# Kernel optimization log

Measured on AMD Instinct MI355X. Metric: run time of the kernel, lower is better.

## Reference

```python
import jax, jax.numpy as jnp
import numpy as np

EPS = 1e-7
ROUTING_ITERS = 3

def squash(s, axis=-1):
    # v = (|s|^2 / (1+|s|^2)) * s / |s|
    sq = jnp.sum(jnp.square(s), axis=axis, keepdims=True)
    return (sq / (1.0 + sq)) * s / jnp.sqrt(sq + EPS)

def setup_inputs() -> dict:
    key = jax.random.key(0)
    k1, k2 = jax.random.split(key)
    B, NI, DI = 64, 2048, 8      # batch, input capsules, input capsule dim
    NC, DC = 32, 16              # output capsules, output capsule dim
    x = jax.random.normal(k1, (B, NI, DI), dtype=jnp.float32)
    W = jax.random.normal(k2, (NC, NI, DC, DI), dtype=jnp.float32) * 0.05
    return {"x": x, "W": W}

def reference(x, W):
    # x: [B, NI, DI], W: [NC, NI, DC, DI]
    # tf.einsum('iabc,abdc->iabd') == project each input capsule per output capsule
    u = jnp.einsum('bif,cidf->bcid', x, W)          # [B, NC, NI, DC]
    B, NC, NI, DC = u.shape
    b = jnp.zeros((B, NC, NI, 1), dtype=u.dtype)
    v = None
    for _ in range(ROUTING_ITERS):
        c = jax.nn.softmax(b, axis=1)                # coupling over output capsules
        s = jnp.sum(c * u, axis=2, keepdims=True)    # [B, NC, 1, DC]
        v = squash(s, axis=-1)                       # [B, NC, 1, DC]
        # original: reduce_sum(matmul(u, tile(v)^T), axis=3) == NI * <u_i, v>
        agree = jnp.sum(u * v, axis=-1, keepdims=True)  # [B, NC, NI, 1]
        b = b + NI * agree
    return jnp.squeeze(v, axis=2)                    # [B, NC, DC]
```

## Files before the change

### kernel.cpp

```cpp
#include <hip/hip_runtime.h>

#define NI 2048
#define NB 64
#define NC 32
#define DC 16
#define DI 8

static constexpr float SQ_EPS = 1e-7f;

typedef float f8 __attribute__((ext_vector_type(8)));

template <int MODE>
__global__
__attribute__((amdgpu_flat_work_group_size(256, 256), amdgpu_waves_per_eu(2, 2)))
void route_pass(
    const float* __restrict__ x, const float* __restrict__ W,
    const float* __restrict__ veff, float* __restrict__ partial)
{
    __shared__ float4 wbuf[2112];

    const int tid   = threadIdx.x;
    const int wave  = tid >> 6;
    const int lane  = tid & 63;
    const int c     = lane & 31;
    const int dg    = lane >> 5;
    const int brel0 = wave * 4;
    const int b0    = blockIdx.y * 16 + brel0;

    f8 s0 = {}, s1 = {}, s2 = {}, s3 = {};

    f8 va = {}, vb = {}, vc = {}, vd = {};
    if (MODE == 1) {
        va = *reinterpret_cast<const f8*>(veff + (((size_t)(b0+0)*2 + dg)*32 + c)*8);
        vb = *reinterpret_cast<const f8*>(veff + (((size_t)(b0+1)*2 + dg)*32 + c)*8);
        vc = *reinterpret_cast<const f8*>(veff + (((size_t)(b0+2)*2 + dg)*32 + c)*8);
        vd = *reinterpret_cast<const f8*>(veff + (((size_t)(b0+3)*2 + dg)*32 + c)*8);
    }

    for (int rnd = 0; rnd < 8; ++rnd) {
        const int i0 = blockIdx.x * 16 + rnd * 2;
        __syncthreads();
        {
            const int k   = tid & 31;
            const int p0  = tid >> 5;
            const int k10 = k & 15, kdg = k >> 4;
#pragma unroll
            for (int r = 0; r < 8; ++r) {
                const int row = r * 8 + p0;
                const int cc  = row >> 1;
                const int sub = row & 1;
                wbuf[((sub * 16 + k10) * 2 + kdg) * 33 + cc] =
                    reinterpret_cast<const float4*>(W)[
                        ((size_t)cc * NI + i0 + sub) * 32 + k];
            }
        }
        __syncthreads();

#pragma unroll
        for (int il = 0; il < 2; ++il) {
            const f8 xav = *reinterpret_cast<const f8*>(
                x + ((size_t)(b0+0) * NI + i0 + il) * 8);
            const f8 xbv = *reinterpret_cast<const f8*>(
                x + ((size_t)(b0+1) * NI + i0 + il) * 8);
            const f8 xcv = *reinterpret_cast<const f8*>(
                x + ((size_t)(b0+2) * NI + i0 + il) * 8);
            const f8 xdv = *reinterpret_cast<const f8*>(
                x + ((size_t)(b0+3) * NI + i0 + il) * 8);

            f8 u0 = {}, u1 = {}, u2 = {}, u3 = {};
#pragma unroll
            for (int dd = 0; dd < 8; ++dd) {
                const float4 wl = wbuf[((il*16 + dd*2    )*2 + dg)*33 + c];
                const float4 wh = wbuf[((il*16 + dd*2 + 1)*2 + dg)*33 + c];
                u0[dd] = wl.x*xav[0] + wl.y*xav[1] + wl.z*xav[2] + wl.w*xav[3]
                       + wh.x*xav[4] + wh.y*xav[5] + wh.z*xav[6] + wh.w*xav[7];
                u1[dd] = wl.x*xbv[0] + wl.y*xbv[1] + wl.z*xbv[2] + wl.w*xbv[3]
                       + wh.x*xbv[4] + wh.y*xbv[5] + wh.z*xbv[6] + wh.w*xbv[7];
                u2[dd] = wl.x*xcv[0] + wl.y*xcv[1] + wl.z*xcv[2] + wl.w*xcv[3]
                       + wh.x*xcv[4] + wh.y*xcv[5] + wh.z*xcv[6] + wh.w*xcv[7];
                u3[dd] = wl.x*xdv[0] + wl.y*xdv[1] + wl.z*xdv[2] + wl.w*xdv[3]
                       + wh.x*xdv[4] + wh.y*xdv[5] + wh.z*xdv[6] + wh.w*xdv[7];
            }

            if (MODE == 0) {
                const float cu = 1.0f / 32.0f;
                s0 += u0 * cu; s1 += u1 * cu; s2 += u2 * cu; s3 += u3 * cu;
            } else {
#pragma unroll
                for (int pr = 0; pr < 2; ++pr) {
                    const f8& ue = pr ? u2 : u0;
                    const f8& uo = pr ? u3 : u1;
                    const f8& ve = pr ? vc : va;
                    const f8& vo = pr ? vd : vb;
                    float pe = 0.0f, po = 0.0f;
#pragma unroll
                    for (int k = 0; k < 8; ++k) {
                        pe += ue[k] * ve[k];
                        po += uo[k] * vo[k];
                    }
                    const float send = (dg == 0) ? po : pe;
                    const float recv = __shfl_xor(send, 32);
                    float a = ((dg == 0) ? pe : po) + recv;
                    float m = a;
#pragma unroll
                    for (int off = 16; off >= 1; off >>= 1)
                        m = fmaxf(m, __shfl_xor(m, off));
                    const float e = __expf(a - m);
                    float t = e;
#pragma unroll
                    for (int off = 16; off >= 1; off >>= 1)
                        t += __shfl_xor(t, off);
                    const float mine  = e / t;
                    const float other = __shfl_xor(mine, 32);
                    const float ce = (dg == 0) ? mine : other;
                    const float co = (dg == 0) ? other : mine;
                    if (pr == 0) { s0 += u0 * ce; s1 += u1 * co; }
                    else         { s2 += u2 * ce; s3 += u3 * co; }
                }
            }
        }
    }

    {
        const int pblk = blockIdx.y * gridDim.x + blockIdx.x;
        float* gp = partial +
            (((size_t)pblk * 16 + brel0) * 128 + dg * 64 + c * 2) * 4;
        *reinterpret_cast<f8*>(gp)        = s0;
        *reinterpret_cast<f8*>(gp +  512) = s1;
        *reinterpret_cast<f8*>(gp + 1024) = s2;
        *reinterpret_cast<f8*>(gp + 1536) = s3;
    }
}

__global__ __launch_bounds__(512) void reduce_squash(
    const float* __restrict__ partial, float* __restrict__ veff,
    float* __restrict__ out, int phase)
{
    __shared__ float4 red[512];
    const int b   = blockIdx.x;
    const int sub = threadIdx.x & 127;
    const int ibq = threadIdx.x >> 7;
    const int c   = (sub >> 2) & 31;
    const int dq  = sub & 3;

    const float* base = partial
        + ((size_t)(b >> 4) * 2048 + (b & 15)) * 512
        + (dq >> 1) * 256 + c * 8 + (dq & 1) * 4
        + (size_t)ibq * 32 * 8192;
    float4 acc = make_float4(0.f, 0.f, 0.f, 0.f);
#pragma unroll 8
    for (int ib = 0; ib < 32; ++ib) {
        const float4 p = *reinterpret_cast<const float4*>(base + (size_t)ib * 8192);
        acc.x += p.x; acc.y += p.y; acc.z += p.z; acc.w += p.w;
    }
    red[threadIdx.x] = acc;
    __syncthreads();
    if (threadIdx.x < 128) {
        const float4 a1 = red[sub + 128];
        const float4 a2 = red[sub + 256];
        const float4 a3 = red[sub + 384];
        acc.x += a1.x + a2.x + a3.x;
        acc.y += a1.y + a2.y + a3.y;
        acc.z += a1.z + a2.z + a3.z;
        acc.w += a1.w + a2.w + a3.w;

        float sq = acc.x*acc.x + acc.y*acc.y + acc.z*acc.z + acc.w*acc.w;
        sq += __shfl_xor(sq, 1);
        sq += __shfl_xor(sq, 2);
        const float scale = sq / ((1.0f + sq) * sqrtf(sq + SQ_EPS));

        if (phase == 3) {
            float4* op = reinterpret_cast<float4*>(out + ((size_t)b * NC + c) * DC + dq * 4);
            *op = make_float4(scale*acc.x, scale*acc.y, scale*acc.z, scale*acc.w);
        } else {
            const float ns = scale * (float)NI;
            float4* vp = reinterpret_cast<float4*>(
                veff + (((size_t)b * 2 + (dq >> 1)) * 32 + c) * 8 + (dq & 1) * 4);
            if (phase == 1) {
                *vp = make_float4(ns*acc.x, ns*acc.y, ns*acc.z, ns*acc.w);
            } else {
                float4 old = *vp;
                *vp = make_float4(old.x + ns*acc.x, old.y + ns*acc.y,
                                  old.z + ns*acc.z, old.w + ns*acc.w);
            }
        }
    }
}

extern "C" void kernel_launch(void* const* d_in, const int* in_sizes, int n_in,
                              void* d_out, int out_size, void* d_ws, size_t ws_size,
                              hipStream_t stream) {
    (void)in_sizes; (void)n_in; (void)out_size; (void)ws_size;
    const float* x = (const float*)d_in[0];
    const float* W = (const float*)d_in[1];

    float* partial = (float*)d_ws;
    float* veff    = (float*)d_out;

    const dim3 grid(128, 4);

    route_pass<0><<<grid, 256, 0, stream>>>(x, W, nullptr, partial);
    reduce_squash<<<64, 512, 0, stream>>>(partial, veff, nullptr, 1);

    route_pass<1><<<grid, 256, 0, stream>>>(x, W, veff, partial);
    reduce_squash<<<64, 512, 0, stream>>>(partial, veff, nullptr, 2);

    route_pass<1><<<grid, 256, 0, stream>>>(x, W, veff, partial);
    reduce_squash<<<64, 512, 0, stream>>>(partial, nullptr, (float*)d_out, 3);
}
```

Baseline: 220.9 us.

## Read W directly from global memory and stage x tile in LDS

The route pass no longer stages the W tile through a padded LDS buffer with per-round barriers. Each lane now reads its 64 W floats per input capsule straight from global memory as 32-byte vectors. The 16x16 block of x vectors is loaded once into LDS and shared by all waves. This removes eight barrier/LDS-transpose rounds, at the cost of uncoalesced strided W reads: each lane touches a different output-capsule row, so every wave load spans many cache lines. Occupancy hints are also relaxed.

```diff
diff --git a/kernel.cpp b/kernel.cpp
--- a/kernel.cpp
+++ b/kernel.cpp
@@ -12,12 +12,12 @@
 
 template <int MODE>
 __global__
-__attribute__((amdgpu_flat_work_group_size(256, 256), amdgpu_waves_per_eu(2, 2)))
+__attribute__((amdgpu_flat_work_group_size(256, 256), amdgpu_waves_per_eu(1, 2)))
 void route_pass(
     const float* __restrict__ x, const float* __restrict__ W,
     const float* __restrict__ veff, float* __restrict__ partial)
 {
-    __shared__ float4 wbuf[2112];
+    __shared__ f8 xbuf[256];
 
     const int tid   = threadIdx.x;
     const int wave  = tid >> 6;
@@ -26,6 +26,7 @@
     const int dg    = lane >> 5;
     const int brel0 = wave * 4;
     const int b0    = blockIdx.y * 16 + brel0;
+    const int i0    = blockIdx.x * 16;
 
     f8 s0 = {}, s1 = {}, s2 = {}, s3 = {};
 
@@ -37,86 +38,74 @@
         vd = *reinterpret_cast<const f8*>(veff + (((size_t)(b0+3)*2 + dg)*32 + c)*8);
     }
 
-    for (int rnd = 0; rnd < 8; ++rnd) {
-        const int i0 = blockIdx.x * 16 + rnd * 2;
-        __syncthreads();
-        {
-            const int k   = tid & 31;
-            const int p0  = tid >> 5;
-            const int k10 = k & 15, kdg = k >> 4;
+    {
+        float4* xb4 = reinterpret_cast<float4*>(xbuf);
+        const float4* xg = reinterpret_cast<const float4*>(x);
+        const int t0 = tid, t1 = tid + 256;
+        xb4[t0] = xg[((size_t)(blockIdx.y*16 + (t0>>5)) * NI + i0)*2 + (t0&31)];
+        xb4[t1] = xg[((size_t)(blockIdx.y*16 + (t1>>5)) * NI + i0)*2 + (t1&31)];
+    }
+    __syncthreads();
+
+    const float* wbase = W + ((size_t)c * NI + i0) * 128 + dg * 64;
+
+#pragma unroll 2
+    for (int ii = 0; ii < 16; ++ii) {
+        const float* wp = wbase + (size_t)ii * 128;
+        const f8 xa = xbuf[(brel0+0)*16 + ii];
+        const f8 xb = xbuf[(brel0+1)*16 + ii];
+        const f8 xc = xbuf[(brel0+2)*16 + ii];
+        const f8 xd = xbuf[(brel0+3)*16 + ii];
+
+        f8 u0 = {}, u1 = {}, u2 = {}, u3 = {};
 #pragma unroll
-            for (int r = 0; r < 8; ++r) {
-                const int row = r * 8 + p0;
-                const int cc  = row >> 1;
-                const int sub = row & 1;
-                wbuf[((sub * 16 + k10) * 2 + kdg) * 33 + cc] =
-                    reinterpret_cast<const float4*>(W)[
-                        ((size_t)cc * NI + i0 + sub) * 32 + k];
+        for (int dd = 0; dd < 8; ++dd) {
+            const f8 wv = *reinterpret_cast<const f8*>(wp + dd * 8);
+            float a0 = 0.f, a1 = 0.f, a2 = 0.f, a3 = 0.f;
+#pragma unroll
+            for (int j = 0; j < 8; ++j) {
+                a0 += wv[j] * xa[j];
+                a1 += wv[j] * xb[j];
+                a2 += wv[j] * xc[j];
+                a3 += wv[j] * xd[j];
             }
+            u0[dd] = a0; u1[dd] = a1; u2[dd] = a2; u3[dd] = a3;
         }
-        __syncthreads();
 
+        if (MODE == 0) {
+            const float cu = 1.0f / 32.0f;
+            s0 += u0 * cu; s1 += u1 * cu; s2 += u2 * cu; s3 += u3 * cu;
+        } else {
 #pragma unroll
-        for (int il = 0; il < 2; ++il) {
-            const f8 xav = *reinterpret_cast<const f8*>(
-                x + ((size_t)(b0+0) * NI + i0 + il) * 8);
-            const f8 xbv = *reinterpret_cast<const f8*>(
-                x + ((size_t)(b0+1) * NI + i0 + il) * 8);
-            const f8 xcv = *reinterpret_cast<const f8*>(
-                x + ((size_t)(b0+2) * NI + i0 + il) * 8);
-            const f8 xdv = *reinterpret_cast<const f8*>(
-                x + ((size_t)(b0+3) * NI + i0 + il) * 8);
-
-            f8 u0 = {}, u1 = {}, u2 = {}, u3 = {};
+            for (int pr = 0; pr < 2; ++pr) {
+                const f8& ue = pr ? u2 : u0;
+                const f8& uo = pr ? u3 : u1;
+                const f8& ve = pr ? vc : va;
+                const f8& vo = pr ? vd : vb;
+                float pe = 0.0f, po = 0.0f;
 #pragma unroll
-            for (int dd = 0; dd < 8; ++dd) {
-                const float4 wl = wbuf[((il*16 + dd*2    )*2 + dg)*33 + c];
-                const float4 wh = wbuf[((il*16 + dd*2 + 1)*2 + dg)*33 + c];
-                u0[dd] = wl.x*xav[0] + wl.y*xav[1] + wl.z*xav[2] + wl.w*xav[3]
-                       + wh.x*xav[4] + wh.y*xav[5] + wh.z*xav[6] + wh.w*xav[7];
-                u1[dd] = wl.x*xbv[0] + wl.y*xbv[1] + wl.z*xbv[2] + wl.w*xbv[3]
-                       + wh.x*xbv[4] + wh.y*xbv[5] + wh.z*xbv[6] + wh.w*xbv[7];
-                u2[dd] = wl.x*xcv[0] + wl.y*xcv[1] + wl.z*xcv[2] + wl.w*xcv[3]
-                       + wh.x*xcv[4] + wh.y*xcv[5] + wh.z*xcv[6] + wh.w*xcv[7];
-                u3[dd] = wl.x*xdv[0] + wl.y*xdv[1] + wl.z*xdv[2] + wl.w*xdv[3]
-                       + wh.x*xdv[4] + wh.y*xdv[5] + wh.z*xdv[6] + wh.w*xdv[7];
-            }
-
-            if (MODE == 0) {
-                const float cu = 1.0f / 32.0f;
-                s0 += u0 * cu; s1 += u1 * cu; s2 += u2 * cu; s3 += u3 * cu;
-            } else {
+                for (int k = 0; k < 8; ++k) {
+                    pe += ue[k] * ve[k];
+                    po += uo[k] * vo[k];
+                }
+                const float send = (dg == 0) ? po : pe;
+                const float recv = __shfl_xor(send, 32);
+                float a = ((dg == 0) ? pe : po) + recv;
+                float m = a;
 #pragma unroll
-                for (int pr = 0; pr < 2; ++pr) {
-                    const f8& ue = pr ? u2 : u0;
-                    const f8& uo = pr ? u3 : u1;
-                    const f8& ve = pr ? vc : va;
-                    const f8& vo = pr ? vd : vb;
-                    float pe = 0.0f, po = 0.0f;
+                for (int off = 16; off >= 1; off >>= 1)
+                    m = fmaxf(m, __shfl_xor(m, off));
+                const float e = __expf(a - m);
+                float t = e;
 #pragma unroll
-                    for (int k = 0; k < 8; ++k) {
-                        pe += ue[k] * ve[k];
-                        po += uo[k] * vo[k];
-                    }
-                    const float send = (dg == 0) ? po : pe;
-                    const float recv = __shfl_xor(send, 32);
-                    float a = ((dg == 0) ? pe : po) + recv;
-                    float m = a;
-#pragma unroll
-                    for (int off = 16; off >= 1; off >>= 1)
-                        m = fmaxf(m, __shfl_xor(m, off));
-                    const float e = __expf(a - m);
-                    float t = e;
-#pragma unroll
-                    for (int off = 16; off >= 1; off >>= 1)
-                        t += __shfl_xor(t, off);
-                    const float mine  = e / t;
-                    const float other = __shfl_xor(mine, 32);
-                    const float ce = (dg == 0) ? mine : other;
-                    const float co = (dg == 0) ? other : mine;
-                    if (pr == 0) { s0 += u0 * ce; s1 += u1 * co; }
-                    else         { s2 += u2 * ce; s3 += u3 * co; }
-                }
+                for (int off = 16; off >= 1; off >>= 1)
+                    t += __shfl_xor(t, off);
+                const float mine  = e / t;
+                const float other = __shfl_xor(mine, 32);
+                const float ce = (dg == 0) ? mine : other;
+                const float co = (dg == 0) ? other : mine;
+                if (pr == 0) { s0 += u0 * ce; s1 += u1 * co; }
+                else         { s2 += u2 * ce; s3 += u3 * co; }
             }
         }
     }
```

After: 276.7 us. 25.3% more time.
